# Kernel tuning notes

Measured on AMD Instinct MI355X. Metric: run time of the kernel, lower is better.

Reference implementation:

```python
import jax, jax.numpy as jnp
import numpy as np

SEQ_LEN = 64  # config.SEQ_LEN
T, B, N, D = 256, 128, 4, 2
H_HIS, H_INT = 32, 8


def _uniform(key, shape, k):
    return jax.random.uniform(key, shape, jnp.float32, -k, k)


def setup_inputs() -> dict:
    key = jax.random.key(0)
    ks = jax.random.split(key, 12)
    kh = 1.0 / np.sqrt(H_HIS)
    ki = 1.0 / np.sqrt(H_INT)
    ko = 1.0 / np.sqrt(40)
    return {
        "inputs": jax.random.normal(ks[0], (T, B, N, D), jnp.float32),
        # history LSTM (input 2 -> hidden 32), gate order i,f,g,o like torch
        "Wih_his": _uniform(ks[1], (4 * H_HIS, D), kh),
        "Whh_his": _uniform(ks[2], (4 * H_HIS, H_HIS), kh),
        "bih_his": _uniform(ks[3], (4 * H_HIS,), kh),
        "bhh_his": _uniform(ks[4], (4 * H_HIS,), kh),
        # interaction LSTM (input 2 -> hidden 8)
        "Wih_int": _uniform(ks[5], (4 * H_INT, D), ki),
        "Whh_int": _uniform(ks[6], (4 * H_INT, H_INT), ki),
        "bih_int": _uniform(ks[7], (4 * H_INT,), ki),
        "bhh_int": _uniform(ks[8], (4 * H_INT,), ki),
        # output Linear(40 -> 2)
        "W_out": _uniform(ks[9], (2, H_HIS + H_INT), ko),
        "b_out": _uniform(ks[10], (2,), ko),
    }


def _lstm_windows(x_w, valid, Wih, Whh, bih, bhh):
    """Run an LSTM over L steps for T independent windows at once.
    x_w: [L, Tw, B, d]  inputs per step (leading padding for short windows)
    valid: [L, Tw] bool; while False the state is held at zero, which is
    exactly equivalent to starting the window fresh at its first valid step.
    Returns final hidden state h: [Tw, B, H].
    """
    H = Whh.shape[1]
    Tw, Bb = x_w.shape[1], x_w.shape[2]
    b = bih + bhh

    def step(carry, xs):
        h, c = carry
        x, v = xs
        g = x @ Wih.T + h @ Whh.T + b            # [Tw, B, 4H]
        i, f, gg, o = jnp.split(g, 4, axis=-1)
        c_new = jax.nn.sigmoid(f) * c + jax.nn.sigmoid(i) * jnp.tanh(gg)
        h_new = jax.nn.sigmoid(o) * jnp.tanh(c_new)
        m = v[:, None, None]
        return (jnp.where(m, h_new, 0.0), jnp.where(m, c_new, 0.0)), None

    init = (jnp.zeros((Tw, Bb, H), x_w.dtype), jnp.zeros((Tw, Bb, H), x_w.dtype))
    (h, _), _ = jax.lax.scan(step, init, (x_w, valid))
    return h


def reference(inputs, Wih_his, Whh_his, bih_his, bhh_his,
              Wih_int, Whh_int, bih_int, bhh_int, W_out, b_out):
    Tt, Bb, Nn, Dd = inputs.shape
    L = SEQ_LEN
    # window index for output frame t: frames t-L+1 .. t (clipped; invalid masked)
    t = jnp.arange(Tt)[:, None]
    s = jnp.arange(L)[None, :]
    idx = t - (L - 1) + s                      # [T, L]
    valid = (idx >= 0)
    idx_c = jnp.clip(idx, 0, Tt - 1)
    x_his = inputs[:, :, -1, :][idx_c]         # [T, L, B, d] (ego / last node)
    x_int = inputs[:, :, 0, :][idx_c]          # [T, L, B, d] (interaction node)
    x_his = jnp.transpose(x_his, (1, 0, 2, 3))  # [L, T, B, d]
    x_int = jnp.transpose(x_int, (1, 0, 2, 3))
    v = jnp.transpose(valid)                   # [L, T]

    h_his = _lstm_windows(x_his, v, Wih_his, Whh_his, bih_his, bhh_his)  # [T,B,32]
    h_int = _lstm_windows(x_int, v, Wih_int, Whh_int, bih_int, bhh_int)  # [T,B,8]
    emb = jnp.concatenate([h_his, h_int], axis=-1)                       # [T,B,40]
    return emb @ W_out.T + b_out                                         # [T,B,2]
```

## Files before the change

kernel.cpp:

```cpp
#include <hip/hip_runtime.h>


typedef float v4f __attribute__((ext_vector_type(4)));
typedef _Float16 h8v __attribute__((ext_vector_type(8)));

static __device__ __forceinline__ float fexp2(float x) {
    return __builtin_amdgcn_exp2f(x);
}
static __device__ __forceinline__ float frcp(float x) {
    return __builtin_amdgcn_rcpf(x);
}
static __device__ __forceinline__ unsigned short f2h(float f) {
    _Float16 h = (_Float16)f;
    unsigned short u;
    __builtin_memcpy(&u, &h, 2);
    return u;
}
static __device__ __forceinline__ float h2f(unsigned short u) {
    _Float16 h;
    __builtin_memcpy(&h, &u, 2);
    return (float)h;
}

#define LOG2E    1.442695041f
#define TWOLOG2E 2.885390082f
#define H16ONE   0x3C00u

__global__ __launch_bounds__(256) void prep_kernel(
    const float* __restrict__ Wih_his, const float* __restrict__ Whh_his,
    const float* __restrict__ bih_his, const float* __restrict__ bhh_his,
    const float* __restrict__ Wih_int, const float* __restrict__ Whh_int,
    const float* __restrict__ bih_int, const float* __restrict__ bhh_int,
    float* __restrict__ ws)
{
    const int i = blockIdx.x * 256 + threadIdx.x;
    unsigned short* wsu = reinterpret_cast<unsigned short*>(ws);

    if (i < 4096) {
        const int T = i >> 9, m = (i >> 5) & 15, k = i & 31;
        const int g = T >> 1;
        const int u = ((m >> 2) << 3) + ((T & 1) << 2) + (m & 3);
        const int orig = g * 32 + u;
        const float s = (g == 2) ? -TWOLOG2E : -LOG2E;
        wsu[i] = f2h(Whh_his[orig * 32 + k] * s);
    } else if (i < 8192) {
        const int e = i - 4096;
        const int T = e >> 9, m = (e >> 5) & 15, k = e & 31;
        const int g = T >> 1;
        const int u = ((m >> 2) << 3) + ((T & 1) << 2) + (m & 3);
        const int orig = g * 32 + u;
        const float s = (g == 2) ? -TWOLOG2E : -LOG2E;
        const float w0 = Wih_his[orig * 2] * s;
        const float w1 = Wih_his[orig * 2 + 1] * s;
        const float b  = (bih_his[orig] + bhh_his[orig]) * s;
        unsigned short v = 0;
        switch (k) {
            case 0: v = f2h(w0); break;
            case 1: v = f2h(w1); break;
            case 2: v = f2h(b);  break;
            case 3: v = f2h(w0 - h2f(f2h(w0))); break;
            case 4: v = f2h(w1 - h2f(f2h(w1))); break;
            case 5: v = f2h(b  - h2f(f2h(b)));  break;
            case 6: v = f2h(w0); break;
            case 7: v = f2h(w1); break;
            default: v = 0; break;
        }
        wsu[4096 + e] = v;
    } else if (i < 9216) {
        const int e = i - 8192;
        const int T = e >> 9, m = (e >> 5) & 15, k = e & 31;
        const int q = k >> 3, j = k & 7;
        const int g = 2 * T + ((m & 3) >> 1);
        const int u = 2 * (m >> 2) + (m & 1);
        const int orig = g * 8 + u;
        const float s = (g == 2) ? -TWOLOG2E : -LOG2E;
        unsigned short v = 0;
        if (j < 6) {
            const int col = 2 * q + (j & 1);
            const float w = Whh_int[orig * 8 + col] * s;
            v = (j == 2 || j == 3) ? f2h(w - h2f(f2h(w))) : f2h(w);
        } else {
            const int comp = j & 1;
            if (q <= 1) {
                v = f2h(Wih_int[orig * 2 + comp] * s);
            } else if (q == 2) {
                const float w = Wih_int[orig * 2 + comp] * s;
                v = f2h(w - h2f(f2h(w)));
            } else {
                const float b = (bih_int[orig] + bhh_int[orig]) * s;
                v = (comp == 0) ? f2h(b) : f2h(b - h2f(f2h(b)));
            }
        }
        wsu[8192 + e] = v;
    }
}

__global__ __launch_bounds__(64) void intw_kernel(
    const float* __restrict__ inp, const float* __restrict__ ws,
    const float* __restrict__ W_out, float* __restrict__ eInt)
{
    const int lane = threadIdx.x;
    const int n    = lane & 15;
    const int q    = lane >> 4;
    const int Wd   = blockIdx.x;
    const int t    = Wd >> 3;
    const int bg   = Wd & 7;
    const int nsteps = (t >= 63) ? 64 : (t + 1);
    const int tau0   = (t >= 63) ? (t - 63) : 0;

    const unsigned short* wsu = reinterpret_cast<const unsigned short*>(ws);
    const h8v* wa = reinterpret_cast<const h8v*>(wsu + 8192);
    h8v AI[2];
#pragma unroll
    for (int T = 0; T < 2; ++T) AI[T] = wa[T * 64 + n * 4 + q];

    const int chain = bg * 16 + n;
    const float* xp = inp + tau0 * 1024 + chain * 8;
    float2 xv = *reinterpret_cast<const float2*>(xp);
    xp += 1024;

    union BU { unsigned u[4]; h8v h; } bh;
    bh.u[0] = bh.u[1] = bh.u[2] = bh.u[3] = 0;

    float cI0 = 0.f, cI1 = 0.f, ih0 = 0.f, ih1 = 0.f;

#pragma unroll 1
    for (int s = 0; s < nsteps; ++s) {
        float2 xn = make_float2(0.f, 0.f);
        if (s + 1 < nsteps)
            xn = *reinterpret_cast<const float2*>(xp);
        xp += 1024;

        {
            const unsigned short xh = f2h(xv.x), yh = f2h(xv.y);
            const unsigned short xl = f2h(xv.x - h2f(xh));
            const unsigned short yl = f2h(xv.y - h2f(yh));
            const unsigned pkh = ((unsigned)yh << 16) | xh;
            const unsigned pkl = ((unsigned)yl << 16) | xl;
            bh.u[3] = (q == 3) ? ((H16ONE << 16) | H16ONE)
                               : ((q == 1) ? pkl : pkh);
        }

        const v4f z = {0.f, 0.f, 0.f, 0.f};
        const v4f D0 = __builtin_amdgcn_mfma_f32_16x16x32_f16(AI[0], bh.h, z, 0, 0, 0);
        const v4f D1 = __builtin_amdgcn_mfma_f32_16x16x32_f16(AI[1], bh.h, z, 0, 0, 0);

        {
            const float si = frcp(1.f + fexp2(D0[0]));
            const float sf = frcp(1.f + fexp2(D0[2]));
            const float tg = fmaf(2.f, frcp(1.f + fexp2(D1[0])), -1.f);
            const float so = frcp(1.f + fexp2(D1[2]));
            const float cn = fmaf(sf, cI0, si * tg);
            cI0 = cn;
            ih0 = so * fmaf(-2.f, frcp(1.f + fexp2(TWOLOG2E * cn)), 1.f);
        }
        {
            const float si = frcp(1.f + fexp2(D0[1]));
            const float sf = frcp(1.f + fexp2(D0[3]));
            const float tg = fmaf(2.f, frcp(1.f + fexp2(D1[1])), -1.f);
            const float so = frcp(1.f + fexp2(D1[3]));
            const float cn = fmaf(sf, cI1, si * tg);
            cI1 = cn;
            ih1 = so * fmaf(-2.f, frcp(1.f + fexp2(TWOLOG2E * cn)), 1.f);
        }

        {
            const unsigned short hh0 = f2h(ih0), hh1 = f2h(ih1);
            const unsigned short hl0 = f2h(ih0 - h2f(hh0));
            const unsigned short hl1 = f2h(ih1 - h2f(hh1));
            bh.u[0] = ((unsigned)hh1 << 16) | hh0;
            bh.u[1] = bh.u[0];
            bh.u[2] = ((unsigned)hl1 << 16) | hl0;
        }

        xv = xn;
    }

    const float wo0a = W_out[32 + 2 * q], wo0b = W_out[33 + 2 * q];
    const float wo1a = W_out[72 + 2 * q], wo1b = W_out[73 + 2 * q];
    float e0 = fmaf(wo0b, ih1, wo0a * ih0);
    float e1 = fmaf(wo1b, ih1, wo1a * ih0);
    e0 += __shfl_xor(e0, 16); e1 += __shfl_xor(e1, 16);
    e0 += __shfl_xor(e0, 32); e1 += __shfl_xor(e1, 32);
    if (lane < 16) {
        float2 o; o.x = e0; o.y = e1;
        reinterpret_cast<float2*>(eInt)[t * 128 + chain] = o;
    }
}

__global__ __launch_bounds__(64) void hisw_kernel(
    const float* __restrict__ inp, const float* __restrict__ ws,
    const float* __restrict__ W_out, const float* __restrict__ b_out,
    const float* __restrict__ eInt, float* __restrict__ out)
{
    const int lane = threadIdx.x;
    const int n    = lane & 15;
    const int q    = lane >> 4;
    const int Wd   = blockIdx.x;
    const int t    = Wd >> 3;
    const int bg   = Wd & 7;
    const int nsteps = (t >= 63) ? 64 : (t + 1);
    const int tau0   = (t >= 63) ? (t - 63) : 0;

    const unsigned short* wsu = reinterpret_cast<const unsigned short*>(ws);
    const h8v* wa = reinterpret_cast<const h8v*>(wsu);
    const h8v* wx = reinterpret_cast<const h8v*>(wsu + 4096);
    h8v AW[8], AX[8];
#pragma unroll
    for (int T = 0; T < 8; ++T) {
        AW[T] = wa[T * 64 + n * 4 + q];
        AX[T] = wx[T * 64 + n * 4 + q];
    }

    const int chain = bg * 16 + n;
    const float* xp = inp + tau0 * 1024 + chain * 8 + 6;
    float2 xv = *reinterpret_cast<const float2*>(xp);
    xp += 1024;

    union BU { unsigned u[4]; h8v h; } bh;
    bh.u[0] = bh.u[1] = bh.u[2] = bh.u[3] = 0;
    float c[8] = {0.f, 0.f, 0.f, 0.f, 0.f, 0.f, 0.f, 0.f};
    float h[8] = {0.f, 0.f, 0.f, 0.f, 0.f, 0.f, 0.f, 0.f};

#pragma unroll 1
    for (int s = 0; s < nsteps; ++s) {
        float2 xn = make_float2(0.f, 0.f);
        if (s + 1 < nsteps)
            xn = *reinterpret_cast<const float2*>(xp);
        xp += 1024;

        union BU bx;
        {
            const unsigned short xh = f2h(xv.x), yh = f2h(xv.y);
            const unsigned short xl = f2h(xv.x - h2f(xh));
            const unsigned short yl = f2h(xv.y - h2f(yh));
            bx.u[0] = ((unsigned)yh << 16) | xh;
            bx.u[1] = ((unsigned)xh << 16) | H16ONE;
            bx.u[2] = (H16ONE << 16) | yh;
            bx.u[3] = ((unsigned)yl << 16) | xl;
            if (q != 0) { bx.u[0] = 0; bx.u[1] = 0; bx.u[2] = 0; bx.u[3] = 0; }
        }

        const v4f z = {0.f, 0.f, 0.f, 0.f};
        v4f D[8];
#pragma unroll
        for (int T = 0; T < 8; ++T) {
            const v4f cx = __builtin_amdgcn_mfma_f32_16x16x32_f16(AX[T], bx.h, z, 0, 0, 0);
            D[T] = __builtin_amdgcn_mfma_f32_16x16x32_f16(AW[T], bh.h, cx, 0, 0, 0);
        }

#pragma unroll
        for (int hi = 0; hi < 2; ++hi) {
#pragma unroll
            for (int lo = 0; lo < 4; ++lo) {
                const int ww = hi * 4 + lo;
                const float si = frcp(1.f + fexp2(D[hi][lo]));
                const float sf = frcp(1.f + fexp2(D[2 + hi][lo]));
                const float tg = fmaf(2.f, frcp(1.f + fexp2(D[4 + hi][lo])), -1.f);
                const float so = frcp(1.f + fexp2(D[6 + hi][lo]));
                const float cn = fmaf(sf, c[ww], si * tg);
                c[ww] = cn;
                h[ww] = so * fmaf(-2.f, frcp(1.f + fexp2(TWOLOG2E * cn)), 1.f);
            }
        }

#pragma unroll
        for (int d = 0; d < 4; ++d)
            bh.u[d] = ((unsigned)f2h(h[2 * d + 1]) << 16) | f2h(h[2 * d]);

        xv = xn;
    }

    const v4f w0a = *reinterpret_cast<const v4f*>(W_out + q * 8);
    const v4f w0b = *reinterpret_cast<const v4f*>(W_out + q * 8 + 4);
    const v4f w1a = *reinterpret_cast<const v4f*>(W_out + 40 + q * 8);
    const v4f w1b = *reinterpret_cast<const v4f*>(W_out + 40 + q * 8 + 4);
    float e0 = 0.f, e1 = 0.f;
#pragma unroll
    for (int j = 0; j < 4; ++j) {
        e0 = fmaf(w0a[j], h[j], fmaf(w0b[j], h[4 + j], e0));
        e1 = fmaf(w1a[j], h[j], fmaf(w1b[j], h[4 + j], e1));
    }
    e0 += __shfl_xor(e0, 16); e1 += __shfl_xor(e1, 16);
    e0 += __shfl_xor(e0, 32); e1 += __shfl_xor(e1, 32);

    if (lane < 16) {
        const float2 ei = reinterpret_cast<const float2*>(eInt)[t * 128 + chain];
        float2 o;
        o.x = e0 + ei.x + b_out[0];
        o.y = e1 + ei.y + b_out[1];
        reinterpret_cast<float2*>(out)[t * 128 + chain] = o;
    }
}

extern "C" void kernel_launch(void* const* d_in, const int* in_sizes, int n_in,
                              void* d_out, int out_size, void* d_ws, size_t ws_size,
                              hipStream_t stream) {
    const float* inp     = (const float*)d_in[0];
    const float* Wih_his = (const float*)d_in[1];
    const float* Whh_his = (const float*)d_in[2];
    const float* bih_his = (const float*)d_in[3];
    const float* bhh_his = (const float*)d_in[4];
    const float* Wih_int = (const float*)d_in[5];
    const float* Whh_int = (const float*)d_in[6];
    const float* bih_int = (const float*)d_in[7];
    const float* bhh_int = (const float*)d_in[8];
    const float* W_out   = (const float*)d_in[9];
    const float* b_out   = (const float*)d_in[10];
    float* out  = (float*)d_out;
    float* ws   = (float*)d_ws;
    float* eInt = ws + 8192;

    prep_kernel<<<dim3(36), dim3(256), 0, stream>>>(
        Wih_his, Whh_his, bih_his, bhh_his,
        Wih_int, Whh_int, bih_int, bhh_int, ws);

    intw_kernel<<<dim3(2048), dim3(64), 0, stream>>>(inp, ws, W_out, eInt);

    hisw_kernel<<<dim3(2048), dim3(64), 0, stream>>>(
        inp, ws, W_out, b_out, eInt, out);
}
```

Baseline: 185.9 us.

## Fuse interaction and history LSTM window kernels into one kernel

Merges the interaction-LSTM kernel and the history-LSTM kernel into a single kernel that advances both recurrences in the same step loop, sharing the input loads and the final output projection. This removes one kernel launch, the eInt round trip through global memory, and lets the small interaction MFMAs and activations interleave with the larger history chain to hide latency. In exchange each wave holds more registers (extra A fragments and states), which could lower occupancy and lengthen the per-step critical path.

Measured after the change: 182.6 us. Within noise of the previous version (-1.8%).

```diff
diff --git a/kernel.cpp b/kernel.cpp
--- a/kernel.cpp
+++ b/kernel.cpp
@@ -95,9 +95,10 @@
     }
 }
 
-__global__ __launch_bounds__(64) void intw_kernel(
+__global__ __launch_bounds__(64) void fusedw_kernel(
     const float* __restrict__ inp, const float* __restrict__ ws,
-    const float* __restrict__ W_out, float* __restrict__ eInt)
+    const float* __restrict__ W_out, const float* __restrict__ b_out,
+    float* __restrict__ out)
 {
     const int lane = threadIdx.x;
     const int n    = lane & 15;
@@ -109,144 +110,99 @@
     const int tau0   = (t >= 63) ? (t - 63) : 0;
 
     const unsigned short* wsu = reinterpret_cast<const unsigned short*>(ws);
-    const h8v* wa = reinterpret_cast<const h8v*>(wsu + 8192);
-    h8v AI[2];
-#pragma unroll
-    for (int T = 0; T < 2; ++T) AI[T] = wa[T * 64 + n * 4 + q];
-
-    const int chain = bg * 16 + n;
-    const float* xp = inp + tau0 * 1024 + chain * 8;
-    float2 xv = *reinterpret_cast<const float2*>(xp);
-    xp += 1024;
-
-    union BU { unsigned u[4]; h8v h; } bh;
-    bh.u[0] = bh.u[1] = bh.u[2] = bh.u[3] = 0;
-
-    float cI0 = 0.f, cI1 = 0.f, ih0 = 0.f, ih1 = 0.f;
-
-#pragma unroll 1
-    for (int s = 0; s < nsteps; ++s) {
-        float2 xn = make_float2(0.f, 0.f);
-        if (s + 1 < nsteps)
-            xn = *reinterpret_cast<const float2*>(xp);
-        xp += 1024;
-
-        {
-            const unsigned short xh = f2h(xv.x), yh = f2h(xv.y);
-            const unsigned short xl = f2h(xv.x - h2f(xh));
-            const unsigned short yl = f2h(xv.y - h2f(yh));
-            const unsigned pkh = ((unsigned)yh << 16) | xh;
-            const unsigned pkl = ((unsigned)yl << 16) | xl;
-            bh.u[3] = (q == 3) ? ((H16ONE << 16) | H16ONE)
-                               : ((q == 1) ? pkl : pkh);
-        }
-
-        const v4f z = {0.f, 0.f, 0.f, 0.f};
-        const v4f D0 = __builtin_amdgcn_mfma_f32_16x16x32_f16(AI[0], bh.h, z, 0, 0, 0);
-        const v4f D1 = __builtin_amdgcn_mfma_f32_16x16x32_f16(AI[1], bh.h, z, 0, 0, 0);
-
-        {
-            const float si = frcp(1.f + fexp2(D0[0]));
-            const float sf = frcp(1.f + fexp2(D0[2]));
-            const float tg = fmaf(2.f, frcp(1.f + fexp2(D1[0])), -1.f);
-            const float so = frcp(1.f + fexp2(D1[2]));
-            const float cn = fmaf(sf, cI0, si * tg);
-            cI0 = cn;
-            ih0 = so * fmaf(-2.f, frcp(1.f + fexp2(TWOLOG2E * cn)), 1.f);
-        }
-        {
-            const float si = frcp(1.f + fexp2(D0[1]));
-            const float sf = frcp(1.f + fexp2(D0[3]));
-            const float tg = fmaf(2.f, frcp(1.f + fexp2(D1[1])), -1.f);
-            const float so = frcp(1.f + fexp2(D1[3]));
-            const float cn = fmaf(sf, cI1, si * tg);
-            cI1 = cn;
-            ih1 = so * fmaf(-2.f, frcp(1.f + fexp2(TWOLOG2E * cn)), 1.f);
-        }
-
-        {
-            const unsigned short hh0 = f2h(ih0), hh1 = f2h(ih1);
-            const unsigned short hl0 = f2h(ih0 - h2f(hh0));
-            const unsigned short hl1 = f2h(ih1 - h2f(hh1));
-            bh.u[0] = ((unsigned)hh1 << 16) | hh0;
-            bh.u[1] = bh.u[0];
-            bh.u[2] = ((unsigned)hl1 << 16) | hl0;
-        }
-
-        xv = xn;
-    }
-
-    const float wo0a = W_out[32 + 2 * q], wo0b = W_out[33 + 2 * q];
-    const float wo1a = W_out[72 + 2 * q], wo1b = W_out[73 + 2 * q];
-    float e0 = fmaf(wo0b, ih1, wo0a * ih0);
-    float e1 = fmaf(wo1b, ih1, wo1a * ih0);
-    e0 += __shfl_xor(e0, 16); e1 += __shfl_xor(e1, 16);
-    e0 += __shfl_xor(e0, 32); e1 += __shfl_xor(e1, 32);
-    if (lane < 16) {
-        float2 o; o.x = e0; o.y = e1;
-        reinterpret_cast<float2*>(eInt)[t * 128 + chain] = o;
-    }
-}
-
-__global__ __launch_bounds__(64) void hisw_kernel(
-    const float* __restrict__ inp, const float* __restrict__ ws,
-    const float* __restrict__ W_out, const float* __restrict__ b_out,
-    const float* __restrict__ eInt, float* __restrict__ out)
-{
-    const int lane = threadIdx.x;
-    const int n    = lane & 15;
-    const int q    = lane >> 4;
-    const int Wd   = blockIdx.x;
-    const int t    = Wd >> 3;
-    const int bg   = Wd & 7;
-    const int nsteps = (t >= 63) ? 64 : (t + 1);
-    const int tau0   = (t >= 63) ? (t - 63) : 0;
-
-    const unsigned short* wsu = reinterpret_cast<const unsigned short*>(ws);
     const h8v* wa = reinterpret_cast<const h8v*>(wsu);
     const h8v* wx = reinterpret_cast<const h8v*>(wsu + 4096);
-    h8v AW[8], AX[8];
+    const h8v* wi = reinterpret_cast<const h8v*>(wsu + 8192);
+    h8v AW[8], AX[8], AI[2];
 #pragma unroll
     for (int T = 0; T < 8; ++T) {
         AW[T] = wa[T * 64 + n * 4 + q];
         AX[T] = wx[T * 64 + n * 4 + q];
     }
+#pragma unroll
+    for (int T = 0; T < 2; ++T) AI[T] = wi[T * 64 + n * 4 + q];
 
     const int chain = bg * 16 + n;
-    const float* xp = inp + tau0 * 1024 + chain * 8 + 6;
-    float2 xv = *reinterpret_cast<const float2*>(xp);
-    xp += 1024;
-
-    union BU { unsigned u[4]; h8v h; } bh;
-    bh.u[0] = bh.u[1] = bh.u[2] = bh.u[3] = 0;
-    float c[8] = {0.f, 0.f, 0.f, 0.f, 0.f, 0.f, 0.f, 0.f};
-    float h[8] = {0.f, 0.f, 0.f, 0.f, 0.f, 0.f, 0.f, 0.f};
+    const float* xb = inp + tau0 * 1024 + chain * 8;
+    float2 xvH = *reinterpret_cast<const float2*>(xb + 6);
+    float2 xvI = *reinterpret_cast<const float2*>(xb);
+    xb += 1024;
+
+    union BU { unsigned u[4]; h8v h; };
+    BU bhH; bhH.u[0] = bhH.u[1] = bhH.u[2] = bhH.u[3] = 0;
+    BU bhI; bhI.u[0] = bhI.u[1] = bhI.u[2] = bhI.u[3] = 0;
+    float cH[8] = {0.f, 0.f, 0.f, 0.f, 0.f, 0.f, 0.f, 0.f};
+    float hH[8] = {0.f, 0.f, 0.f, 0.f, 0.f, 0.f, 0.f, 0.f};
+    float cI0 = 0.f, cI1 = 0.f, ih0 = 0.f, ih1 = 0.f;
 
 #pragma unroll 1
     for (int s = 0; s < nsteps; ++s) {
-        float2 xn = make_float2(0.f, 0.f);
-        if (s + 1 < nsteps)
-            xn = *reinterpret_cast<const float2*>(xp);
-        xp += 1024;
-
-        union BU bx;
-        {
-            const unsigned short xh = f2h(xv.x), yh = f2h(xv.y);
-            const unsigned short xl = f2h(xv.x - h2f(xh));
-            const unsigned short yl = f2h(xv.y - h2f(yh));
+        float2 xnH = make_float2(0.f, 0.f);
+        float2 xnI = make_float2(0.f, 0.f);
+        if (s + 1 < nsteps) {
+            xnH = *reinterpret_cast<const float2*>(xb + 6);
+            xnI = *reinterpret_cast<const float2*>(xb);
+        }
+        xb += 1024;
+
+        BU bx;
+        {
+            const unsigned short xh = f2h(xvH.x), yh = f2h(xvH.y);
+            const unsigned short xl = f2h(xvH.x - h2f(xh));
+            const unsigned short yl = f2h(xvH.y - h2f(yh));
             bx.u[0] = ((unsigned)yh << 16) | xh;
             bx.u[1] = ((unsigned)xh << 16) | H16ONE;
             bx.u[2] = (H16ONE << 16) | yh;
             bx.u[3] = ((unsigned)yl << 16) | xl;
             if (q != 0) { bx.u[0] = 0; bx.u[1] = 0; bx.u[2] = 0; bx.u[3] = 0; }
         }
+        {
+            const unsigned short xh = f2h(xvI.x), yh = f2h(xvI.y);
+            const unsigned short xl = f2h(xvI.x - h2f(xh));
+            const unsigned short yl = f2h(xvI.y - h2f(yh));
+            const unsigned ph = ((unsigned)yh << 16) | xh;
+            const unsigned pl = ((unsigned)yl << 16) | xl;
+            bhI.u[3] = (q == 3) ? ((H16ONE << 16) | H16ONE)
+                                : ((q == 1) ? pl : ph);
+        }
 
         const v4f z = {0.f, 0.f, 0.f, 0.f};
+
+        const v4f E0 = __builtin_amdgcn_mfma_f32_16x16x32_f16(AI[0], bhI.h, z, 0, 0, 0);
+        const v4f E1 = __builtin_amdgcn_mfma_f32_16x16x32_f16(AI[1], bhI.h, z, 0, 0, 0);
+
         v4f D[8];
 #pragma unroll
         for (int T = 0; T < 8; ++T) {
             const v4f cx = __builtin_amdgcn_mfma_f32_16x16x32_f16(AX[T], bx.h, z, 0, 0, 0);
-            D[T] = __builtin_amdgcn_mfma_f32_16x16x32_f16(AW[T], bh.h, cx, 0, 0, 0);
+            D[T] = __builtin_amdgcn_mfma_f32_16x16x32_f16(AW[T], bhH.h, cx, 0, 0, 0);
+        }
+
+        {
+            const float si = frcp(1.f + fexp2(E0[0]));
+            const float sf = frcp(1.f + fexp2(E0[2]));
+            const float tg = fmaf(2.f, frcp(1.f + fexp2(E1[0])), -1.f);
+            const float so = frcp(1.f + fexp2(E1[2]));
+            const float cn = fmaf(sf, cI0, si * tg);
+            cI0 = cn;
+            ih0 = so * fmaf(-2.f, frcp(1.f + fexp2(TWOLOG2E * cn)), 1.f);
+        }
+        {
+            const float si = frcp(1.f + fexp2(E0[1]));
+            const float sf = frcp(1.f + fexp2(E0[3]));
+            const float tg = fmaf(2.f, frcp(1.f + fexp2(E1[1])), -1.f);
+            const float so = frcp(1.f + fexp2(E1[3]));
+            const float cn = fmaf(sf, cI1, si * tg);
+            cI1 = cn;
+            ih1 = so * fmaf(-2.f, frcp(1.f + fexp2(TWOLOG2E * cn)), 1.f);
+        }
+        {
+            const unsigned short hh0 = f2h(ih0), hh1 = f2h(ih1);
+            const unsigned short hl0 = f2h(ih0 - h2f(hh0));
+            const unsigned short hl1 = f2h(ih1 - h2f(hh1));
+            bhI.u[0] = ((unsigned)hh1 << 16) | hh0;
+            bhI.u[1] = bhI.u[0];
+            bhI.u[2] = ((unsigned)hl1 << 16) | hl0;
         }
 
 #pragma unroll
@@ -258,37 +214,37 @@
                 const float sf = frcp(1.f + fexp2(D[2 + hi][lo]));
                 const float tg = fmaf(2.f, frcp(1.f + fexp2(D[4 + hi][lo])), -1.f);
                 const float so = frcp(1.f + fexp2(D[6 + hi][lo]));
-                const float cn = fmaf(sf, c[ww], si * tg);
-                c[ww] = cn;
-                h[ww] = so * fmaf(-2.f, frcp(1.f + fexp2(TWOLOG2E * cn)), 1.f);
+                const float cn = fmaf(sf, cH[ww], si * tg);
+                cH[ww] = cn;
+                hH[ww] = so * fmaf(-2.f, frcp(1.f + fexp2(TWOLOG2E * cn)), 1.f);
             }
         }
-
 #pragma unroll
         for (int d = 0; d < 4; ++d)
-            bh.u[d] = ((unsigned)f2h(h[2 * d + 1]) << 16) | f2h(h[2 * d]);
-
-        xv = xn;
+            bhH.u[d] = ((unsigned)f2h(hH[2 * d + 1]) << 16) | f2h(hH[2 * d]);
+
+        xvH = xnH;
+        xvI = xnI;
     }
 
     const v4f w0a = *reinterpret_cast<const v4f*>(W_out + q * 8);
     const v4f w0b = *reinterpret_cast<const v4f*>(W_out + q * 8 + 4);
     const v4f w1a = *reinterpret_cast<const v4f*>(W_out + 40 + q * 8);
     const v4f w1b = *reinterpret_cast<const v4f*>(W_out + 40 + q * 8 + 4);
-    float e0 = 0.f, e1 = 0.f;
+    float e0 = fmaf(W_out[33 + 2 * q], ih1, W_out[32 + 2 * q] * ih0);
+    float e1 = fmaf(W_out[73 + 2 * q], ih1, W_out[72 + 2 * q] * ih0);
 #pragma unroll
     for (int j = 0; j < 4; ++j) {
-        e0 = fmaf(w0a[j], h[j], fmaf(w0b[j], h[4 + j], e0));
-        e1 = fmaf(w1a[j], h[j], fmaf(w1b[j], h[4 + j], e1));
+        e0 = fmaf(w0a[j], hH[j], fmaf(w0b[j], hH[4 + j], e0));
+        e1 = fmaf(w1a[j], hH[j], fmaf(w1b[j], hH[4 + j], e1));
     }
     e0 += __shfl_xor(e0, 16); e1 += __shfl_xor(e1, 16);
     e0 += __shfl_xor(e0, 32); e1 += __shfl_xor(e1, 32);
 
     if (lane < 16) {
-        const float2 ei = reinterpret_cast<const float2*>(eInt)[t * 128 + chain];
         float2 o;
-        o.x = e0 + ei.x + b_out[0];
-        o.y = e1 + ei.y + b_out[1];
+        o.x = e0 + b_out[0];
+        o.y = e1 + b_out[1];
         reinterpret_cast<float2*>(out)[t * 128 + chain] = o;
     }
 }
@@ -309,14 +265,11 @@
     const float* b_out   = (const float*)d_in[10];
     float* out  = (float*)d_out;
     float* ws   = (float*)d_ws;
-    float* eInt = ws + 8192;
 
     prep_kernel<<<dim3(36), dim3(256), 0, stream>>>(
         Wih_his, Whh_his, bih_his, bhh_his,
         Wih_int, Whh_int, bih_int, bhh_int, ws);
 
-    intw_kernel<<<dim3(2048), dim3(64), 0, stream>>>(inp, ws, W_out, eInt);
-
-    hisw_kernel<<<dim3(2048), dim3(64), 0, stream>>>(
-        inp, ws, W_out, b_out, eInt, out);
-}
+    fusedw_kernel<<<dim3(2048), dim3(64), 0, stream>>>(
+        inp, ws, W_out, b_out, out);
+}
```
